# Kernel optimization log

Measured on AMD Instinct MI355X. Metric: run time of the kernel, lower is better.

## Reference

```python
import jax, jax.numpy as jnp
import numpy as np

N_MOLS = 32768        # number of molecules in the batch
N_ATOMS = 4_194_304   # total atoms across all molecules (~128 atoms/mol)


def setup_inputs() -> dict:
    key = jax.random.key(0)
    k1, k2, k3 = jax.random.split(key, 3)
    xyz = jax.random.normal(k1, (N_ATOMS, 3), dtype=jnp.float32)
    # sorted segment ids == torch.split by per-molecule counts
    segment_ids = jnp.sort(jax.random.randint(k2, (N_ATOMS,), 0, N_MOLS))
    # minimal differentiable per-atom energy head (stand-in for upstream net)
    w = jax.random.normal(k3, (3,), dtype=jnp.float32)
    return {"xyz": xyz, "segment_ids": segment_ids, "w": w}


def reference(xyz, segment_ids, w):
    # atomwise energy: [N_ATOMS]; segment-sum -> per-molecule energy [N_MOLS]
    def energy_fn(x):
        atomwise = jnp.tanh(x @ w)
        return jax.ops.segment_sum(atomwise, segment_ids, num_segments=N_MOLS)

    energy, vjp_fn = jax.vjp(energy_fn, xyz)
    # compute_grad(output=energy, inputs=xyz) with ones grad_outputs
    (energy_grad,) = vjp_fn(jnp.ones_like(energy))
    return energy, energy_grad
```

## Files before the change

kernel.cpp:

```cpp
#include <hip/hip_runtime.h>

#define N_MOLS   32768
#define NATOMS   4194304
#define BLOCK    256
#define APT      4
#define APB      (BLOCK * APT)
#define NBINS    1088

__device__ __forceinline__ void add_seg(float* bins, float* energy,
                                        int first_id, int id, float v) {
    int local = id - first_id;
    if (local < NBINS) {
        atomicAdd(&bins[local], v);
    } else {
        atomicAdd(&energy[id], v);
    }
}

__global__ __launch_bounds__(BLOCK)
void SumPool_5325759447404_kernel(const float* __restrict__ xyz,
                                  const int*   __restrict__ seg,
                                  const float* __restrict__ w,
                                  float* __restrict__ energy,
                                  float* __restrict__ grad) {
    __shared__ float bins[NBINS];
    const int block_start = blockIdx.x * APB;

    for (int i = threadIdx.x; i < NBINS; i += BLOCK) bins[i] = 0.0f;

    const float w0 = w[0], w1 = w[1], w2 = w[2];
    const int first_id = seg[block_start];
    __syncthreads();

    const int a0 = block_start + threadIdx.x * APT;

    const float4* __restrict__ xyz4 = (const float4*)(xyz + (size_t)a0 * 3);
    const float4 p = xyz4[0];
    const float4 q = xyz4[1];
    const float4 r = xyz4[2];

    const float s0 = p.x * w0 + p.y * w1 + p.z * w2;
    const float s1 = p.w * w0 + q.x * w1 + q.y * w2;
    const float s2 = q.z * w0 + q.w * w1 + r.x * w2;
    const float s3 = r.y * w0 + r.z * w1 + r.w * w2;

    const float t0 = tanhf(s0);
    const float t1 = tanhf(s1);
    const float t2 = tanhf(s2);
    const float t3 = tanhf(s3);

    const float d0 = 1.0f - t0 * t0;
    const float d1 = 1.0f - t1 * t1;
    const float d2 = 1.0f - t2 * t2;
    const float d3 = 1.0f - t3 * t3;

    float4 g0, g1, g2;
    g0.x = d0 * w0; g0.y = d0 * w1; g0.z = d0 * w2; g0.w = d1 * w0;
    g1.x = d1 * w1; g1.y = d1 * w2; g1.z = d2 * w0; g1.w = d2 * w1;
    g2.x = d2 * w2; g2.y = d3 * w0; g2.z = d3 * w1; g2.w = d3 * w2;

    float4* __restrict__ grad4 = (float4*)(grad + (size_t)a0 * 3);
    grad4[0] = g0;
    grad4[1] = g1;
    grad4[2] = g2;

    const int4 ids = *(const int4*)(seg + a0);

    float acc = t0;
    int   cur = ids.x;
    if (ids.y == cur) { acc += t1; } else { add_seg(bins, energy, first_id, cur, acc); cur = ids.y; acc = t1; }
    if (ids.z == cur) { acc += t2; } else { add_seg(bins, energy, first_id, cur, acc); cur = ids.z; acc = t2; }
    if (ids.w == cur) { acc += t3; } else { add_seg(bins, energy, first_id, cur, acc); cur = ids.w; acc = t3; }
    add_seg(bins, energy, first_id, cur, acc);

    __syncthreads();

    const int last_id = seg[block_start + APB - 1];
    int range = last_id - first_id + 1;
    if (range > NBINS) range = NBINS;
    for (int i = threadIdx.x; i < range; i += BLOCK) {
        const float v = bins[i];
        if (v != 0.0f) atomicAdd(&energy[first_id + i], v);
    }
}

extern "C" void kernel_launch(void* const* d_in, const int* in_sizes, int n_in,
                              void* d_out, int out_size, void* d_ws, size_t ws_size,
                              hipStream_t stream) {
    const float* xyz = (const float*)d_in[0];
    const int*   seg = (const int*)d_in[1];
    const float* w   = (const float*)d_in[2];

    float* energy = (float*)d_out;
    float* grad   = energy + N_MOLS;

    hipMemsetAsync(d_out, 0, N_MOLS * sizeof(float), stream);

    const int nblocks = NATOMS / APB;
    SumPool_5325759447404_kernel<<<nblocks, BLOCK, 0, stream>>>(xyz, seg, w, energy, grad);
}
```

Baseline: 116.8 us.

## Replace LDS bin reduction with wavefront segmented scan and fast tanh

Drops the shared-memory bins, both block barriers and the bin flush loop. Each thread's trailing partial sum is now combined across the 64-lane wavefront with a shuffle-based segmented scan, and one global atomic is issued per segment run per wave. tanhf is replaced with an exp plus hardware reciprocal approximation, and xyz loads and grad stores use nontemporal hints. This should remove barrier and LDS overhead, at the cost of more global atomics and slightly lower tanh accuracy.

```diff
diff --git a/kernel.cpp b/kernel.cpp
--- a/kernel.cpp
+++ b/kernel.cpp
@@ -5,16 +5,13 @@
 #define BLOCK    256
 #define APT      4
 #define APB      (BLOCK * APT)
-#define NBINS    1088
 
-__device__ __forceinline__ void add_seg(float* bins, float* energy,
-                                        int first_id, int id, float v) {
-    int local = id - first_id;
-    if (local < NBINS) {
-        atomicAdd(&bins[local], v);
-    } else {
-        atomicAdd(&energy[id], v);
-    }
+typedef float  f32x4 __attribute__((ext_vector_type(4)));
+typedef int    i32x4 __attribute__((ext_vector_type(4)));
+
+__device__ __forceinline__ float fast_tanh(float x) {
+    float e = __expf(2.0f * x);
+    return 1.0f - 2.0f * __builtin_amdgcn_rcpf(e + 1.0f);
 }
 
 __global__ __launch_bounds__(BLOCK)
@@ -23,65 +20,55 @@
                                   const float* __restrict__ w,
                                   float* __restrict__ energy,
                                   float* __restrict__ grad) {
-    __shared__ float bins[NBINS];
-    const int block_start = blockIdx.x * APB;
-
-    for (int i = threadIdx.x; i < NBINS; i += BLOCK) bins[i] = 0.0f;
+    const int a0   = (blockIdx.x * BLOCK + threadIdx.x) * APT;
+    const int lane = threadIdx.x & 63;
 
     const float w0 = w[0], w1 = w[1], w2 = w[2];
-    const int first_id = seg[block_start];
-    __syncthreads();
 
-    const int a0 = block_start + threadIdx.x * APT;
+    const f32x4* __restrict__ xyz4 = (const f32x4*)(xyz + (size_t)a0 * 3);
+    const f32x4 p = __builtin_nontemporal_load(xyz4 + 0);
+    const f32x4 q = __builtin_nontemporal_load(xyz4 + 1);
+    const f32x4 r = __builtin_nontemporal_load(xyz4 + 2);
 
-    const float4* __restrict__ xyz4 = (const float4*)(xyz + (size_t)a0 * 3);
-    const float4 p = xyz4[0];
-    const float4 q = xyz4[1];
-    const float4 r = xyz4[2];
-
-    const float s0 = p.x * w0 + p.y * w1 + p.z * w2;
-    const float s1 = p.w * w0 + q.x * w1 + q.y * w2;
-    const float s2 = q.z * w0 + q.w * w1 + r.x * w2;
-    const float s3 = r.y * w0 + r.z * w1 + r.w * w2;
-
-    const float t0 = tanhf(s0);
-    const float t1 = tanhf(s1);
-    const float t2 = tanhf(s2);
-    const float t3 = tanhf(s3);
+    const float t0 = fast_tanh(p.x * w0 + p.y * w1 + p.z * w2);
+    const float t1 = fast_tanh(p.w * w0 + q.x * w1 + q.y * w2);
+    const float t2 = fast_tanh(q.z * w0 + q.w * w1 + r.x * w2);
+    const float t3 = fast_tanh(r.y * w0 + r.z * w1 + r.w * w2);
 
     const float d0 = 1.0f - t0 * t0;
     const float d1 = 1.0f - t1 * t1;
     const float d2 = 1.0f - t2 * t2;
     const float d3 = 1.0f - t3 * t3;
 
-    float4 g0, g1, g2;
+    f32x4 g0, g1, g2;
     g0.x = d0 * w0; g0.y = d0 * w1; g0.z = d0 * w2; g0.w = d1 * w0;
     g1.x = d1 * w1; g1.y = d1 * w2; g1.z = d2 * w0; g1.w = d2 * w1;
     g2.x = d2 * w2; g2.y = d3 * w0; g2.z = d3 * w1; g2.w = d3 * w2;
 
-    float4* __restrict__ grad4 = (float4*)(grad + (size_t)a0 * 3);
-    grad4[0] = g0;
-    grad4[1] = g1;
-    grad4[2] = g2;
+    f32x4* __restrict__ grad4 = (f32x4*)(grad + (size_t)a0 * 3);
+    __builtin_nontemporal_store(g0, grad4 + 0);
+    __builtin_nontemporal_store(g1, grad4 + 1);
+    __builtin_nontemporal_store(g2, grad4 + 2);
 
-    const int4 ids = *(const int4*)(seg + a0);
+    const i32x4 ids = *(const i32x4*)(seg + a0);
 
     float acc = t0;
     int   cur = ids.x;
-    if (ids.y == cur) { acc += t1; } else { add_seg(bins, energy, first_id, cur, acc); cur = ids.y; acc = t1; }
-    if (ids.z == cur) { acc += t2; } else { add_seg(bins, energy, first_id, cur, acc); cur = ids.z; acc = t2; }
-    if (ids.w == cur) { acc += t3; } else { add_seg(bins, energy, first_id, cur, acc); cur = ids.w; acc = t3; }
-    add_seg(bins, energy, first_id, cur, acc);
+    if (ids.y == cur) { acc += t1; } else { atomicAdd(&energy[cur], acc); cur = ids.y; acc = t1; }
+    if (ids.z == cur) { acc += t2; } else { atomicAdd(&energy[cur], acc); cur = ids.z; acc = t2; }
+    if (ids.w == cur) { acc += t3; } else { atomicAdd(&energy[cur], acc); cur = ids.w; acc = t3; }
 
-    __syncthreads();
-
-    const int last_id = seg[block_start + APB - 1];
-    int range = last_id - first_id + 1;
-    if (range > NBINS) range = NBINS;
-    for (int i = threadIdx.x; i < range; i += BLOCK) {
-        const float v = bins[i];
-        if (v != 0.0f) atomicAdd(&energy[first_id + i], v);
+    float v  = acc;
+    int   id = cur;
+    #pragma unroll
+    for (int off = 1; off < 64; off <<= 1) {
+        float vv = __shfl_up(v, off, 64);
+        int   ii = __shfl_up(id, off, 64);
+        if (lane >= off && ii == id) v += vv;
     }
+    const int nid   = __shfl_down(id, 1, 64);
+    const bool last = (lane == 63) || (nid != id);
+    if (last) atomicAdd(&energy[id], v);
 }
 
 extern "C" void kernel_launch(void* const* d_in, const int* in_sizes, int n_in,
@@ -94,7 +81,7 @@
     float* energy = (float*)d_out;
     float* grad   = energy + N_MOLS;
 
-    hipMemsetAsync(d_out, 0, N_MOLS * sizeof(float), stream);
+    (void)hipMemsetAsync(d_out, 0, N_MOLS * sizeof(float), stream);
 
     const int nblocks = NATOMS / APB;
     SumPool_5325759447404_kernel<<<nblocks, BLOCK, 0, stream>>>(xyz, seg, w, energy, grad);
```

Measured after the change: 123.2 us. 1.06x slower.
